# Optimization experiments

Measured on AMD Instinct MI355X. Metric: run time of the kernel, lower is better.

The kernel has to match this reference:

```python
import jax, jax.numpy as jnp
import numpy as np
from jax import lax

B, T, V, D, HD, H = 64, 256, 50000, 300, 1024, 512
L0, L1 = 13, 25


def setup_inputs() -> dict:
    key = jax.random.key(0)
    ks = list(jax.random.split(key, 24))
    lengths = jnp.concatenate([jnp.array([T]), jax.random.randint(ks[0], (B - 1,), T // 2, T + 1)])
    ids = jax.random.randint(ks[1], (B, T), 1, V)
    pos = jnp.arange(T)[None, :]
    word_batch = jnp.where(pos < lengths[:, None], ids, 0)
    def nrm(k, shape, s):
        return jax.random.normal(k, shape, dtype=jnp.float32) * s
    sc = 1.0 / float(np.sqrt(H))
    return dict(
        word_batch=word_batch,
        emb=nrm(ks[2], (V, D), 0.1),
        lstm0_wih=nrm(ks[3], (2, 4 * H, D), sc),
        lstm0_whh=nrm(ks[4], (2, 4 * H, H), sc),
        lstm0_b=nrm(ks[5], (2, 4 * H), sc),
        lstm1_wih=nrm(ks[6], (2, 4 * H, HD), sc),
        lstm1_whh=nrm(ks[7], (2, 4 * H, H), sc),
        lstm1_b=nrm(ks[8], (2, 4 * H), sc),
        head0_w=nrm(ks[9], (L0, HD), 0.02),
        head0_b=jnp.zeros((L0,), jnp.float32),
        head1_w=nrm(ks[10], (L1, HD + 1), 0.02),
        head1_b=jnp.zeros((L1,), jnp.float32),
        crf0_start=nrm(ks[11], (L0,), 0.1),
        crf0_end=nrm(ks[12], (L0,), 0.1),
        crf0_trans=nrm(ks[13], (L0, L0), 0.1),
        crf1_start=nrm(ks[14], (L1,), 0.1),
        crf1_end=nrm(ks[15], (L1,), 0.1),
        crf1_trans=nrm(ks[16], (L1, L1), 0.1),
    )


def reverse_padded(x, lengths):
    # reverse each sequence within its valid length; zeros in the padded tail
    Tn = x.shape[1]
    idx = lengths[:, None] - 1 - jnp.arange(Tn)[None, :]  # [B,T]
    valid = idx >= 0
    g = jnp.take_along_axis(x, jnp.clip(idx, 0)[:, :, None], axis=1)
    return jnp.where(valid[:, :, None], g, 0.0)


def lstm_scan(x, mask, w_ih, w_hh, b):
    # one direction; PyTorch gate order i,f,g,o. Packed-sequence semantics via mask
    Bn = x.shape[0]
    Hn = w_hh.shape[-1]
    xp = jnp.einsum('btd,gd->btg', x, w_ih) + b  # [B,T,4H]
    def step(carry, inp):
        h, c = carry
        gx, m = inp
        g = gx + h @ w_hh.T
        i, f, gg, o = jnp.split(g, 4, axis=-1)
        c_new = jax.nn.sigmoid(f) * c + jax.nn.sigmoid(i) * jnp.tanh(gg)
        h_new = jax.nn.sigmoid(o) * jnp.tanh(c_new)
        m2 = m[:, None]
        h = jnp.where(m2, h_new, h)
        c = jnp.where(m2, c_new, c)
        return (h, c), h * m2
    z = jnp.zeros((Bn, Hn), x.dtype)
    _, ys = lax.scan(step, (z, z), (xp.transpose(1, 0, 2), mask.T))
    return ys.transpose(1, 0, 2)


def bilstm_layer(x, mask, lengths, wih, whh, b):
    f = lstm_scan(x, mask, wih[0], whh[0], b[0])
    r = lstm_scan(reverse_padded(x, lengths), mask, wih[1], whh[1], b[1])
    return jnp.concatenate([f, reverse_padded(r, lengths)], axis=-1)


def viterbi(em, mask, start, end, trans):
    # torchcrf-style Viterbi decode with mask; identity-backpointers on padded steps
    Bn, Tn, Ln = em.shape
    score = start + em[:, 0]  # [B,L]
    iden = jnp.arange(Ln)[None, :]
    def step(score, inp):
        e, m = inp
        br = score[:, :, None] + trans[None]      # [B,Lprev,Lnext]
        nsc = jnp.max(br, axis=1) + e
        idx = jnp.argmax(br, axis=1)
        m2 = m[:, None]
        idx = jnp.where(m2, idx, iden)
        score = jnp.where(m2, nsc, score)
        return score, idx
    score, hist = lax.scan(step, score, (em[:, 1:].transpose(1, 0, 2), mask[:, 1:].T))
    final = score + end
    last = jnp.argmax(final, axis=-1)  # [B]
    best = jnp.max(final, axis=-1)
    def back(tag, h):
        prev = jnp.take_along_axis(h, tag[:, None], axis=1)[:, 0]
        return prev, prev
    _, prevs = lax.scan(back, last, hist, reverse=True)  # [T-1,B]
    tags = jnp.concatenate([prevs, last[None]], axis=0).T  # [B,T]
    return jnp.where(mask, tags, 0), best


def reference(word_batch, emb, lstm0_wih, lstm0_whh, lstm0_b, lstm1_wih, lstm1_whh, lstm1_b,
              head0_w, head0_b, head1_w, head1_b,
              crf0_start, crf0_end, crf0_trans, crf1_start, crf1_end, crf1_trans):
    mask = word_batch > 0
    lengths = mask.sum(axis=1)
    x = emb[word_batch]                                  # [B,T,D]
    out = bilstm_layer(x, mask, lengths, lstm0_wih, lstm0_whh, lstm0_b)
    out = bilstm_layer(out, mask, lengths, lstm1_wih, lstm1_whh, lstm1_b)  # [B,T,HD]
    em0 = out @ head0_w.T + head0_b
    tags0, _ = viterbi(em0, mask, crf0_start, crf0_end, crf0_trans)
    # extend: concat previous decoded tags (padded with 0) as an extra float channel
    ext = jnp.concatenate([out, tags0.astype(jnp.float32)[:, :, None]], axis=-1)
    em1 = ext @ head1_w.T + head1_b
    tags1, _ = viterbi(em1, mask, crf1_start, crf1_end, crf1_trans)
    return jnp.stack([tags0, tags1]), lengths
```

## Files before the change

### kernel.cpp

```cpp
#include <hip/hip_runtime.h>
#include <math.h>

#define B_ 64
#define T_ 256
#define D_ 300
#define H_ 512
#define G4_ 2048
#define HD_ 1024
#define CH_ 64
#define KP0 320

typedef short s8v __attribute__((ext_vector_type(8)));
typedef float f32x4 __attribute__((ext_vector_type(4)));
typedef __attribute__((address_space(1))) const char GChar;
typedef __attribute__((address_space(3))) char LChar;

#define HSWZ(lby, b) ((lby) ^ ((size_t)((b) & 15) << 4))

__device__ inline unsigned short f2bf_rne(float f) {
  unsigned u = __builtin_bit_cast(unsigned, f);
  unsigned r = (u + 0x7fff + ((u >> 16) & 1)) >> 16;
  return (unsigned short)r;
}
__device__ inline float bf2f(unsigned short h) {
  unsigned u = ((unsigned)h) << 16;
  return __builtin_bit_cast(float, u);
}

__device__ inline float fsig(float x) { return 1.f / (1.f + __expf(-x)); }
__device__ inline float ftanh(float x) { return 2.f / (1.f + __expf(-2.f * x)) - 1.f; }

__global__ void k_lengths(const int* __restrict__ word, int* __restrict__ lens,
                          int* __restrict__ out_len) {
  __shared__ int s[256];
  int b = blockIdx.x, t = threadIdx.x;
  s[t] = (word[b * T_ + t] > 0) ? 1 : 0;
  __syncthreads();
  for (int off = 128; off > 0; off >>= 1) {
    if (t < off) s[t] += s[t + off];
    __syncthreads();
  }
  if (t == 0) { lens[b] = s[0]; out_len[b] = s[0]; }
}

__global__ void k_embed_bf(const int* __restrict__ word, const float* __restrict__ emb,
                           unsigned short* __restrict__ xHi, unsigned short* __restrict__ xLo) {
  const int C8 = KP0 / 8;
  int idx = blockIdx.x * blockDim.x + threadIdx.x;
  if (idx >= T_ * B_ * C8) return;
  int d8 = idx % C8;
  int row = idx / C8;
  int b = row % B_, t = row / B_;
  int w = word[b * T_ + t];
  unsigned short hh[8], ll[8];
#pragma unroll
  for (int e = 0; e < 8; e++) {
    int d = d8 * 8 + e;
    float f = (d < D_) ? emb[(size_t)w * D_ + d] : 0.f;
    hh[e] = f2bf_rne(f);
    ll[e] = f2bf_rne(f - bf2f(hh[e]));
  }
  size_t o = (size_t)row * KP0 + d8 * 8;
  ((ushort4*)(xHi + o))[0] = make_ushort4(hh[0], hh[1], hh[2], hh[3]);
  ((ushort4*)(xHi + o))[1] = make_ushort4(hh[4], hh[5], hh[6], hh[7]);
  ((ushort4*)(xLo + o))[0] = make_ushort4(ll[0], ll[1], ll[2], ll[3]);
  ((ushort4*)(xLo + o))[1] = make_ushort4(ll[4], ll[5], ll[6], ll[7]);
}

__global__ void k_split(const float* __restrict__ w, unsigned short* __restrict__ hi,
                        unsigned short* __restrict__ lo, int n) {
  int i = blockIdx.x * blockDim.x + threadIdx.x;
  if (i >= n) return;
  float f = w[i];
  unsigned short h = f2bf_rne(f);
  hi[i] = h;
  lo[i] = f2bf_rne(f - bf2f(h));
}

template <int KP>
__global__ void k_splitw(const float* __restrict__ w, unsigned short* __restrict__ hi,
                         unsigned short* __restrict__ lo, int K) {
  const int C8 = KP / 8;
  int idx = blockIdx.x * blockDim.x + threadIdx.x;
  if (idx >= 2 * G4_ * C8) return;
  int d8 = idx % C8;
  int row = idx / C8;
  unsigned short hh[8], ll[8];
#pragma unroll
  for (int e = 0; e < 8; e++) {
    int d = d8 * 8 + e;
    float f = (d < K) ? w[(size_t)row * K + d] : 0.f;
    hh[e] = f2bf_rne(f);
    ll[e] = f2bf_rne(f - bf2f(hh[e]));
  }
  size_t o = (size_t)row * KP + d8 * 8;
  ((ushort4*)(hi + o))[0] = make_ushort4(hh[0], hh[1], hh[2], hh[3]);
  ((ushort4*)(hi + o))[1] = make_ushort4(hh[4], hh[5], hh[6], hh[7]);
  ((ushort4*)(lo + o))[0] = make_ushort4(ll[0], ll[1], ll[2], ll[3]);
  ((ushort4*)(lo + o))[1] = make_ushort4(ll[4], ll[5], ll[6], ll[7]);
}

template <int KSTEPS>
__global__ __launch_bounds__(256) void k_projg(
    const unsigned short* __restrict__ sHi, const unsigned short* __restrict__ sLo,
    const unsigned short* __restrict__ wHi, const unsigned short* __restrict__ wLo,
    const float* __restrict__ bias, const int* __restrict__ lens,
    float* __restrict__ xpf, float* __restrict__ xpr, int t0,
    const char* __restrict__ zpage) {
  const int KP = KSTEPS * 64;
  int mb = blockIdx.x, nb = blockIdx.y, rev = blockIdx.z;
  int tid = threadIdx.x;
  int w = tid >> 6, lane = tid & 63, lm = lane & 15;
  int wm = w >> 1, wn = w & 1;

  __shared__ char lds[65536];

  const char* aHp[4]; const char* aLp[4]; const char* bHp[4]; const char* bLp[4];
  int c16 = tid & 7;
#pragma unroll
  for (int it = 0; it < 4; it++) {
    int row = it * 32 + (tid >> 3);
    int sw = (c16 * 16) ^ ((row & 7) << 4);
    int grow = mb * 128 + row;
    int b = grow & 63, tl = grow >> 6;
    long srow;
    if (!rev) srow = (long)(t0 + tl) * B_ + b;
    else {
      int tp = lens[b] - 1 - (t0 + tl);
      srow = (tp >= 0) ? ((long)tp * B_ + b) : -1;
    }
    if (srow >= 0) {
      aHp[it] = (const char*)sHi + (size_t)srow * (KP * 2) + sw;
      aLp[it] = (const char*)sLo + (size_t)srow * (KP * 2) + sw;
    } else {
      aHp[it] = zpage + sw;
      aLp[it] = zpage + sw;
    }
    int col = nb * 128 + row;
    size_t wrow = (size_t)rev * G4_ + col;
    bHp[it] = (const char*)wHi + wrow * (KP * 2) + sw;
    bLp[it] = (const char*)wLo + wrow * (KP * 2) + sw;
  }

  f32x4 acc[4][4];
#pragma unroll
  for (int mi = 0; mi < 4; mi++)
#pragma unroll
    for (int ni = 0; ni < 4; ni++) {
      f32x4 z = {0.f, 0.f, 0.f, 0.f};
      acc[mi][ni] = z;
    }

  for (int ks = 0; ks < KSTEPS; ks++) {
    if (ks) __syncthreads();
    int so = ks * 128;
#pragma unroll
    for (int it = 0; it < 4; it++) {
      int o = it * 4096 + tid * 16;
      __builtin_amdgcn_global_load_lds((GChar*)(aHp[it] + so), (LChar*)(lds + o), 16, 0, 0);
      __builtin_amdgcn_global_load_lds((GChar*)(aLp[it] + so), (LChar*)(lds + 16384 + o), 16, 0, 0);
      __builtin_amdgcn_global_load_lds((GChar*)(bHp[it] + so), (LChar*)(lds + 32768 + o), 16, 0, 0);
      __builtin_amdgcn_global_load_lds((GChar*)(bLp[it] + so), (LChar*)(lds + 49152 + o), 16, 0, 0);
    }
    __syncthreads();
#pragma unroll
    for (int ki = 0; ki < 2; ki++) {
      int kb = ki * 64 + (lane >> 4) * 16;
      s8v ahf[4], alf[4], bhf[4], blf[4];
#pragma unroll
      for (int mi = 0; mi < 4; mi++) {
        int row = wm * 64 + mi * 16 + lm;
        int p = row * 128 + (kb ^ ((row & 7) << 4));
        ahf[mi] = *(const s8v*)(lds + p);
        alf[mi] = *(const s8v*)(lds + 16384 + p);
      }
#pragma unroll
      for (int ni = 0; ni < 4; ni++) {
        int row = wn * 64 + ni * 16 + lm;
        int p = row * 128 + (kb ^ ((row & 7) << 4));
        bhf[ni] = *(const s8v*)(lds + 32768 + p);
        blf[ni] = *(const s8v*)(lds + 49152 + p);
      }
#pragma unroll
      for (int mi = 0; mi < 4; mi++)
#pragma unroll
        for (int ni = 0; ni < 4; ni++) {
          acc[mi][ni] = __builtin_amdgcn_mfma_f32_16x16x32_bf16(ahf[mi], bhf[ni], acc[mi][ni], 0, 0, 0);
          acc[mi][ni] = __builtin_amdgcn_mfma_f32_16x16x32_bf16(alf[mi], bhf[ni], acc[mi][ni], 0, 0, 0);
          acc[mi][ni] = __builtin_amdgcn_mfma_f32_16x16x32_bf16(ahf[mi], blf[ni], acc[mi][ni], 0, 0, 0);
        }
    }
  }

  int tl = mb * 2 + wm;
  float* xpo = (rev ? xpr : xpf) + (size_t)tl * G4_ * B_;
#pragma unroll
  for (int ni = 0; ni < 4; ni++) {
    int col = nb * 128 + wn * 64 + ni * 16 + lm;
    float bv = bias[rev * G4_ + col];
    f32x4 bvv = {bv, bv, bv, bv};
#pragma unroll
    for (int mi = 0; mi < 4; mi++) {
      int b0 = mi * 16 + (lane >> 4) * 4;
      f32x4 v = acc[mi][ni] + bvv;
      *(f32x4*)(xpo + (size_t)col * B_ + b0) = v;
    }
  }
}

__global__ __launch_bounds__(512, 2) void k_lstm_chunk(
    const unsigned short* __restrict__ whh_hi, const unsigned short* __restrict__ whh_lo,
    const float* __restrict__ xpf, const float* __restrict__ xpr,
    const int* __restrict__ lens,
    unsigned short* __restrict__ hhi, unsigned short* __restrict__ hlo,
    float* __restrict__ cbuf,
    float* __restrict__ outF, unsigned short* __restrict__ oHi,
    unsigned short* __restrict__ oLo, int t0, int tbase, int mode,
    unsigned* __restrict__ flags) {
  int wg = blockIdx.x;
  int dir = wg >> 5;
  int u0 = (wg & 31) * 16;
  int tid = threadIdx.x;
  int w8 = tid >> 6;
  int g = w8 >> 1;
  int hh = w8 & 1;
  int lane = tid & 63;
  int lm = lane & 15;
  int kb = (lane >> 4) * 16;
  int n = g * H_ + u0 + lm;

  const unsigned short* Whi = whh_hi + (size_t)dir * G4_ * H_;
  const unsigned short* Wlo = whh_lo + (size_t)dir * G4_ * H_;
  const float* xpb = (dir == 0) ? xpf : xpr;

  __shared__ char lbuf[131072];
  float* glx = (float*)lbuf;

  s8v bh[16], bl[16];
#pragma unroll
  for (int kt = 0; kt < 16; kt++) {
    bh[kt] = *(const s8v*)(Whi + (size_t)n * H_ + kt * 32 + (kb >> 1));
    bl[kt] = *(const s8v*)(Wlo + (size_t)n * H_ + kt * 32 + (kb >> 1));
  }

  int eb = tid & 63;
  int uq = tid >> 6;
  int len = lens[eb];
  size_t lby = (size_t)eb * 1024 + (size_t)(u0 + uq * 2) * 2;
  size_t pby = HSWZ(lby, eb);
  size_t coff = ((size_t)dir * B_ + eb) * H_ + u0 + uq * 2;
  float2 cv2 = *(const float2*)(cbuf + coff);
  float creg[2] = {cv2.x, cv2.y};

  float xq[8];
#pragma unroll
  for (int q2 = 0; q2 < 8; q2++) {
    int gg = q2 >> 1, qq = q2 & 1;
    xq[q2] = xpb[(size_t)(gg * H_ + u0 + uq * 2 + qq) * B_ + eb];
  }

  {
    int pp = t0 & 1;
    const char* sH = (const char*)(hhi + (size_t)(pp * 2 + dir) * B_ * H_);
    const char* sL = (const char*)(hlo + (size_t)(pp * 2 + dir) * B_ * H_);
    int sof = w8 * 8192 + lane * 16;
#pragma unroll
    for (int it = 0; it < 8; it++) {
      __builtin_amdgcn_global_load_lds((GChar*)(sH + sof + it * 1024),
                                       (LChar*)(lbuf + sof + it * 1024), 16, 0, 16);
      __builtin_amdgcn_global_load_lds((GChar*)(sL + sof + it * 1024),
                                       (LChar*)(lbuf + 65536 + sof + it * 1024), 16, 0, 16);
    }
  }

  for (int tl = 0; tl < CH_; tl++) {
    int t = t0 + tl;
    int pp = t & 1;
    const char* srcHi = (const char*)(hhi + (size_t)(pp * 2 + dir) * B_ * H_);
    const char* srcLo = (const char*)(hlo + (size_t)(pp * 2 + dir) * B_ * H_);
    char* dstHi = (char*)(hhi + (size_t)((pp ^ 1) * 2 + dir) * B_ * H_);
    char* dstLo = (char*)(hlo + (size_t)((pp ^ 1) * 2 + dir) * B_ * H_);

    __syncthreads();

    f32x4 aH[2], aX[2];
#pragma unroll
    for (int b2 = 0; b2 < 2; b2++) {
      f32x4 z = {0.f, 0.f, 0.f, 0.f};
      aH[b2] = z; aX[b2] = z;
    }
#pragma unroll
    for (int kt = 0; kt < 16; kt++) {
#pragma unroll
      for (int b2 = 0; b2 < 2; b2++) {
        int row = (hh * 2 + b2) * 16 + lm;
        int p = (row * 1024 + kt * 64 + kb) ^ ((lm & 15) << 4);
        s8v ah = *(const s8v*)(lbuf + p);
        s8v al = *(const s8v*)(lbuf + 65536 + p);
        aH[b2] = __builtin_amdgcn_mfma_f32_16x16x32_bf16(ah, bh[kt], aH[b2], 0, 0, 0);
        aX[b2] = __builtin_amdgcn_mfma_f32_16x16x32_bf16(al, bh[kt], aX[b2], 0, 0, 0);
        aX[b2] = __builtin_amdgcn_mfma_f32_16x16x32_bf16(ah, bl[kt], aX[b2], 0, 0, 0);
      }
    }
    __syncthreads();
#pragma unroll
    for (int b2 = 0; b2 < 2; b2++) {
#pragma unroll
      for (int jj = 0; jj < 4; jj++) {
        int brow = (hh * 2 + b2) * 16 + (lane >> 4) * 4 + jj;
        glx[(g * 16 + lm) * 65 + brow] = aH[b2][jj] + aX[b2][jj];
      }
    }
    __syncthreads();

    bool active = (t < len);
    float hn[2];
    ushort2 hi2, lo2;
    if (active) {
#pragma unroll
      for (int q = 0; q < 2; q++) {
        int ul = uq * 2 + q;
        float iv = glx[(0 * 16 + ul) * 65 + eb] + xq[0 * 2 + q];
        float fv = glx[(1 * 16 + ul) * 65 + eb] + xq[1 * 2 + q];
        float gv = glx[(2 * 16 + ul) * 65 + eb] + xq[2 * 2 + q];
        float ov = glx[(3 * 16 + ul) * 65 + eb] + xq[3 * 2 + q];
        float cn = fsig(fv) * creg[q] + fsig(iv) * ftanh(gv);
        creg[q] = cn;
        hn[q] = fsig(ov) * ftanh(cn);
      }
      unsigned short h0 = f2bf_rne(hn[0]); unsigned short l0 = f2bf_rne(hn[0] - bf2f(h0));
      unsigned short h1 = f2bf_rne(hn[1]); unsigned short l1 = f2bf_rne(hn[1] - bf2f(h1));
      hi2.x = h0; hi2.y = h1;
      lo2.x = l0; lo2.y = l1;
      __hip_atomic_store((unsigned*)(dstHi + pby), __builtin_bit_cast(unsigned, hi2),
                         __ATOMIC_RELAXED, __HIP_MEMORY_SCOPE_AGENT);
      __hip_atomic_store((unsigned*)(dstLo + pby), __builtin_bit_cast(unsigned, lo2),
                         __ATOMIC_RELAXED, __HIP_MEMORY_SCOPE_AGENT);
    } else {
      unsigned vh = __hip_atomic_load((const unsigned*)(srcHi + pby),
                                      __ATOMIC_RELAXED, __HIP_MEMORY_SCOPE_AGENT);
      unsigned vl = __hip_atomic_load((const unsigned*)(srcLo + pby),
                                      __ATOMIC_RELAXED, __HIP_MEMORY_SCOPE_AGENT);
      __hip_atomic_store((unsigned*)(dstHi + pby), vh,
                         __ATOMIC_RELAXED, __HIP_MEMORY_SCOPE_AGENT);
      __hip_atomic_store((unsigned*)(dstLo + pby), vl,
                         __ATOMIC_RELAXED, __HIP_MEMORY_SCOPE_AGENT);
    }

    auto do_out = [&]() {
      if (active) {
        size_t orow = (dir == 0) ? ((size_t)t * B_ + eb) : ((size_t)(len - 1 - t) * B_ + eb);
        size_t ocol = (dir == 0) ? (size_t)(u0 + uq * 2) : (size_t)(H_ + u0 + uq * 2);
        if (mode == 0) {
          *(ushort2*)(oHi + orow * HD_ + ocol) = hi2;
          *(ushort2*)(oLo + orow * HD_ + ocol) = lo2;
        } else {
          float2 hv; hv.x = hn[0]; hv.y = hn[1];
          *(float2*)(outF + orow * HD_ + ocol) = hv;
        }
      } else if (dir == 0) {
        size_t o = ((size_t)t * B_ + eb) * HD_ + u0 + uq * 2;
        if (mode == 0) {
          ushort2 z2; z2.x = z2.y = 0;
          *(ushort2*)(oHi + o) = z2;
          *(ushort2*)(oLo + o) = z2;
        } else {
          float2 z; z.x = z.y = 0.f;
          *(float2*)(outF + o) = z;
        }
      }
    };

    if (tl != CH_ - 1) {
      unsigned target = (unsigned)(tbase + t + 1);
      __syncthreads();
      if (tid == 0)
        __hip_atomic_store(flags + wg * 16, target, __ATOMIC_RELAXED, __HIP_MEMORY_SCOPE_AGENT);
      do_out();
#pragma unroll
      for (int q2 = 0; q2 < 8; q2++) {
        int gg = q2 >> 1, qq = q2 & 1;
        xq[q2] = xpb[(size_t)(tl + 1) * G4_ * B_ + (size_t)(gg * H_ + u0 + uq * 2 + qq) * B_ + eb];
      }
      if (tid < 32) {
        const unsigned* p = flags + (dir * 32 + tid) * 16;
        while (true) {
          unsigned v = __hip_atomic_load(p, __ATOMIC_RELAXED, __HIP_MEMORY_SCOPE_AGENT);
          if (__all((int)(v >= target))) break;
        }
      }
      __syncthreads();
      {
        int np = (t + 1) & 1;
        const char* sH = (const char*)(hhi + (size_t)(np * 2 + dir) * B_ * H_);
        const char* sL = (const char*)(hlo + (size_t)(np * 2 + dir) * B_ * H_);
        int sof = w8 * 8192 + lane * 16;
#pragma unroll
        for (int it = 0; it < 8; it++) {
          __builtin_amdgcn_global_load_lds((GChar*)(sH + sof + it * 1024),
                                           (LChar*)(lbuf + sof + it * 1024), 16, 0, 16);
          __builtin_amdgcn_global_load_lds((GChar*)(sL + sof + it * 1024),
                                           (LChar*)(lbuf + 65536 + sof + it * 1024), 16, 0, 16);
        }
      }
    } else {
      do_out();
    }
  }
  *(float2*)(cbuf + coff) = *(const float2*)creg;
}

__global__ void k_em0(const float* __restrict__ o, const float* __restrict__ w,
                      const float* __restrict__ bias, float* __restrict__ em) {
  int gt = blockIdx.x * blockDim.x + threadIdx.x;
  int wid = gt >> 6;
  int lane = threadIdx.x & 63;
  if (wid >= T_ * B_) return;
  const float* row = o + (size_t)wid * HD_;
  float r[16];
#pragma unroll
  for (int q = 0; q < 16; q++) r[q] = row[lane + 64 * q];
  for (int c = 0; c < 13; c++) {
    const float* wr = w + (size_t)c * HD_;
    float p = 0.f;
#pragma unroll
    for (int q = 0; q < 16; q++) p += r[q] * wr[lane + 64 * q];
    for (int off = 32; off > 0; off >>= 1) p += __shfl_down(p, off);
    if (lane == 0) em[(size_t)wid * 16 + c] = p + bias[c];
  }
}

__global__ void k_em1(const float* __restrict__ o, const float* __restrict__ w,
                      const float* __restrict__ bias, const int* __restrict__ tags0,
                      float* __restrict__ em) {
  int gt = blockIdx.x * blockDim.x + threadIdx.x;
  int wid = gt >> 6;
  int lane = threadIdx.x & 63;
  if (wid >= T_ * B_) return;
  int t = wid / B_, b = wid % B_;
  float tag = (float)tags0[b * T_ + t];
  const float* row = o + (size_t)wid * HD_;
  float r[16];
#pragma unroll
  for (int q = 0; q < 16; q++) r[q] = row[lane + 64 * q];
  for (int c = 0; c < 25; c++) {
    const float* wr = w + (size_t)c * 1025;
    float p = 0.f;
#pragma unroll
    for (int q = 0; q < 16; q++) p += r[q] * wr[lane + 64 * q];
    for (int off = 32; off > 0; off >>= 1) p += __shfl_down(p, off);
    if (lane == 0) em[(size_t)wid * 32 + c] = p + wr[1024] * tag + bias[c];
  }
}

template <int L, int LD>
__global__ void k_viterbi(const float* __restrict__ em, const int* __restrict__ lens,
                          const float* __restrict__ startv, const float* __restrict__ endv,
                          const float* __restrict__ trans, int* __restrict__ tags) {
  int b = blockIdx.x;
  int j = threadIdx.x;
  __shared__ float sc[L];
  __shared__ float trT[L * L];
  __shared__ int hist[T_ * LD];
  int len = lens[b];
  if (j < L) {
    sc[j] = startv[j] + em[(size_t)b * LD + j];
    for (int i = 0; i < L; i++) trT[j * L + i] = trans[i * L + j];
  }
  __syncthreads();
  for (int t = 1; t < len; t++) {
    float nv = 0.f; int bi = 0;
    if (j < L) {
      float best = sc[0] + trT[j * L + 0];
      for (int i = 1; i < L; i++) {
        float v = sc[i] + trT[j * L + i];
        if (v > best) { best = v; bi = i; }
      }
      nv = best + em[((size_t)t * B_ + b) * LD + j];
      hist[t * LD + j] = bi;
    }
    __syncthreads();
    if (j < L) sc[j] = nv;
    __syncthreads();
  }
  if (j == 0) {
    float best = sc[0] + endv[0]; int bi = 0;
    for (int i = 1; i < L; i++) {
      float v = sc[i] + endv[i];
      if (v > best) { best = v; bi = i; }
    }
    int tag = bi;
    tags[b * T_ + (len - 1)] = tag;
    for (int t = len - 2; t >= 0; t--) {
      tag = hist[(t + 1) * LD + tag];
      tags[b * T_ + t] = tag;
    }
    for (int t = len; t < T_; t++) tags[b * T_ + t] = 0;
  }
}

extern "C" void kernel_launch(void* const* d_in, const int* in_sizes, int n_in,
                              void* d_out, int out_size, void* d_ws, size_t ws_size,
                              hipStream_t stream) {
  const int*   word = (const int*)d_in[0];
  const float* emb  = (const float*)d_in[1];
  const float* w0ih = (const float*)d_in[2];
  const float* w0hh = (const float*)d_in[3];
  const float* b0   = (const float*)d_in[4];
  const float* w1ih = (const float*)d_in[5];
  const float* w1hh = (const float*)d_in[6];
  const float* b1   = (const float*)d_in[7];
  const float* h0w  = (const float*)d_in[8];
  const float* h0b  = (const float*)d_in[9];
  const float* h1w  = (const float*)d_in[10];
  const float* h1b  = (const float*)d_in[11];
  const float* c0s  = (const float*)d_in[12];
  const float* c0e  = (const float*)d_in[13];
  const float* c0t  = (const float*)d_in[14];
  const float* c1s  = (const float*)d_in[15];
  const float* c1e  = (const float*)d_in[16];
  const float* c1t  = (const float*)d_in[17];

  int* out_tags0 = (int*)d_out;
  int* out_tags1 = out_tags0 + B_ * T_;
  int* out_len   = out_tags1 + B_ * T_;

  char* ws = (char*)d_ws;
  size_t off = 0;
  auto alloc = [&](size_t bytes) -> void* {
    void* p = ws + off;
    off += (bytes + 255) & ~(size_t)255;
    return p;
  };
  int*   lens  = (int*)alloc(B_ * 4);
  unsigned* sync = (unsigned*)alloc(4096);
  char*  zpage = (char*)alloc(4096);
  unsigned short* xHi = (unsigned short*)alloc((size_t)T_ * B_ * KP0 * 2);
  unsigned short* xLo = (unsigned short*)alloc((size_t)T_ * B_ * KP0 * 2);
  unsigned short* oHi = (unsigned short*)alloc((size_t)T_ * B_ * HD_ * 2);
  unsigned short* oLo = (unsigned short*)alloc((size_t)T_ * B_ * HD_ * 2);
  float* out1  = (float*)alloc((size_t)T_ * B_ * HD_ * 4);
  float* xpf   = (float*)alloc((size_t)CH_ * B_ * G4_ * 4);
  float* xpr   = (float*)alloc((size_t)CH_ * B_ * G4_ * 4);
  unsigned short* hhi = (unsigned short*)alloc((size_t)2 * 2 * B_ * H_ * 2);
  unsigned short* hlo = (unsigned short*)alloc((size_t)2 * 2 * B_ * H_ * 2);
  float* cbuf  = (float*)alloc((size_t)2 * B_ * H_ * 4);
  unsigned short* w0hh_hi = (unsigned short*)alloc((size_t)2 * G4_ * H_ * 2);
  unsigned short* w0hh_lo = (unsigned short*)alloc((size_t)2 * G4_ * H_ * 2);
  unsigned short* w1hh_hi = (unsigned short*)alloc((size_t)2 * G4_ * H_ * 2);
  unsigned short* w1hh_lo = (unsigned short*)alloc((size_t)2 * G4_ * H_ * 2);
  unsigned short* w0ih_hi = (unsigned short*)alloc((size_t)2 * G4_ * KP0 * 2);
  unsigned short* w0ih_lo = (unsigned short*)alloc((size_t)2 * G4_ * KP0 * 2);
  unsigned short* w1ih_hi = (unsigned short*)alloc((size_t)2 * G4_ * HD_ * 2);
  unsigned short* w1ih_lo = (unsigned short*)alloc((size_t)2 * G4_ * HD_ * 2);
  float* em0   = (float*)alloc((size_t)T_ * B_ * 16 * 4);
  float* em1   = (float*)alloc((size_t)T_ * B_ * 32 * 4);
  (void)ws_size; (void)in_sizes; (void)n_in; (void)out_size;

  hipMemsetAsync(sync, 0, 4096, stream);
  hipMemsetAsync(zpage, 0, 4096, stream);

  k_lengths<<<B_, 256, 0, stream>>>(word, lens, out_len);
  {
    int total = T_ * B_ * (KP0 / 8);
    k_embed_bf<<<(total + 255) / 256, 256, 0, stream>>>(word, emb, xHi, xLo);
  }
  {
    int n = 2 * G4_ * H_;
    k_split<<<(n + 255) / 256, 256, 0, stream>>>(w0hh, w0hh_hi, w0hh_lo, n);
    k_split<<<(n + 255) / 256, 256, 0, stream>>>(w1hh, w1hh_hi, w1hh_lo, n);
    int n0 = 2 * G4_ * (KP0 / 8);
    k_splitw<KP0><<<(n0 + 255) / 256, 256, 0, stream>>>(w0ih, w0ih_hi, w0ih_lo, D_);
    int n1 = 2 * G4_ * (HD_ / 8);
    k_splitw<HD_><<<(n1 + 255) / 256, 256, 0, stream>>>(w1ih, w1ih_hi, w1ih_lo, HD_);
  }

  for (int layer = 0; layer < 2; layer++) {
    const unsigned short* sHi = (layer == 0) ? xHi : oHi;
    const unsigned short* sLo = (layer == 0) ? xLo : oLo;
    const unsigned short* wiHi = (layer == 0) ? w0ih_hi : w1ih_hi;
    const unsigned short* wiLo = (layer == 0) ? w0ih_lo : w1ih_lo;
    const float* bb  = (layer == 0) ? b0 : b1;
    const unsigned short* whi = (layer == 0) ? w0hh_hi : w1hh_hi;
    const unsigned short* wlo = (layer == 0) ? w0hh_lo : w1hh_lo;
    hipMemsetAsync(hhi, 0, (size_t)2 * 2 * B_ * H_ * 2, stream);
    hipMemsetAsync(hlo, 0, (size_t)2 * 2 * B_ * H_ * 2, stream);
    hipMemsetAsync(cbuf, 0, (size_t)2 * B_ * H_ * 4, stream);
    if (layer == 0) {
      hipMemsetAsync(oHi, 0, (size_t)T_ * B_ * HD_ * 2, stream);
      hipMemsetAsync(oLo, 0, (size_t)T_ * B_ * HD_ * 2, stream);
    } else {
      hipMemsetAsync(out1, 0, (size_t)T_ * B_ * HD_ * 4, stream);
    }
    for (int cch = 0; cch < T_ / CH_; cch++) {
      dim3 pg(CH_ * B_ / 128, G4_ / 128, 2);
      if (layer == 0)
        k_projg<KP0 / 64><<<pg, 256, 0, stream>>>(sHi, sLo, wiHi, wiLo, bb, lens,
                                                  xpf, xpr, cch * CH_, zpage);
      else
        k_projg<HD_ / 64><<<pg, 256, 0, stream>>>(sHi, sLo, wiHi, wiLo, bb, lens,
                                                  xpf, xpr, cch * CH_, zpage);
      k_lstm_chunk<<<64, 512, 0, stream>>>(whi, wlo, xpf, xpr, lens, hhi, hlo,
                                           cbuf, out1, oHi, oLo,
                                           cch * CH_, layer * T_, layer, sync);
    }
  }

  k_em0<<<(T_ * B_) / 4, 256, 0, stream>>>(out1, h0w, h0b, em0);
  k_viterbi<13, 16><<<B_, 64, 0, stream>>>(em0, lens, c0s, c0e, c0t, out_tags0);
  k_em1<<<(T_ * B_) / 4, 256, 0, stream>>>(out1, h1w, h1b, out_tags0, em1);
  k_viterbi<25, 32><<<B_, 64, 0, stream>>>(em1, lens, c1s, c1e, c1t, out_tags1);
}
```

Baseline: 4.469 ms.

## Double LSTM recurrent block to 1024 threads, one batch tile per wave

The recurrent LSTM kernel now launches 1024 threads per block instead of 512. Each of the 16 waves computes a single 16-row batch tile of the h·Whh MFMA product rather than two, which halves the serial MFMA chain per wave on the latency-bound recurrence and halves the per-wave LDS staging loads. Only the first 512 threads run the gate epilogue, the state updates and the output writes. The cost is more idle threads during the epilogue, heavier barriers over 16 waves, and register pressure from keeping the Whh fragments in registers in every wave under the new launch bounds.

```diff
diff --git a/kernel.cpp b/kernel.cpp
--- a/kernel.cpp
+++ b/kernel.cpp
@@ -208,7 +208,7 @@
   }
 }
 
-__global__ __launch_bounds__(512, 2) void k_lstm_chunk(
+__global__ __launch_bounds__(1024, 4) void k_lstm_chunk(
     const unsigned short* __restrict__ whh_hi, const unsigned short* __restrict__ whh_lo,
     const float* __restrict__ xpf, const float* __restrict__ xpr,
     const int* __restrict__ lens,
@@ -221,9 +221,9 @@
   int dir = wg >> 5;
   int u0 = (wg & 31) * 16;
   int tid = threadIdx.x;
-  int w8 = tid >> 6;
-  int g = w8 >> 1;
-  int hh = w8 & 1;
+  int w16 = tid >> 6;
+  int g = w16 >> 2;
+  int bt = w16 & 3;
   int lane = tid & 63;
   int lm = lane & 15;
   int kb = (lane >> 4) * 16;
@@ -244,28 +244,34 @@
   }
 
   int eb = tid & 63;
-  int uq = tid >> 6;
+  int uq = (tid >> 6) & 7;
+  bool epi = (tid < 512);
   int len = lens[eb];
   size_t lby = (size_t)eb * 1024 + (size_t)(u0 + uq * 2) * 2;
   size_t pby = HSWZ(lby, eb);
   size_t coff = ((size_t)dir * B_ + eb) * H_ + u0 + uq * 2;
-  float2 cv2 = *(const float2*)(cbuf + coff);
-  float creg[2] = {cv2.x, cv2.y};
+  float creg[2] = {0.f, 0.f};
+  if (epi) {
+    float2 cv2 = *(const float2*)(cbuf + coff);
+    creg[0] = cv2.x; creg[1] = cv2.y;
+  }
 
   float xq[8];
-#pragma unroll
-  for (int q2 = 0; q2 < 8; q2++) {
-    int gg = q2 >> 1, qq = q2 & 1;
-    xq[q2] = xpb[(size_t)(gg * H_ + u0 + uq * 2 + qq) * B_ + eb];
+  if (epi) {
+#pragma unroll
+    for (int q2 = 0; q2 < 8; q2++) {
+      int gg = q2 >> 1, qq = q2 & 1;
+      xq[q2] = xpb[(size_t)(gg * H_ + u0 + uq * 2 + qq) * B_ + eb];
+    }
   }
 
   {
     int pp = t0 & 1;
     const char* sH = (const char*)(hhi + (size_t)(pp * 2 + dir) * B_ * H_);
     const char* sL = (const char*)(hlo + (size_t)(pp * 2 + dir) * B_ * H_);
-    int sof = w8 * 8192 + lane * 16;
-#pragma unroll
-    for (int it = 0; it < 8; it++) {
+    int sof = w16 * 4096 + lane * 16;
+#pragma unroll
+    for (int it = 0; it < 4; it++) {
       __builtin_amdgcn_global_load_lds((GChar*)(sH + sof + it * 1024),
                                        (LChar*)(lbuf + sof + it * 1024), 16, 0, 16);
       __builtin_amdgcn_global_load_lds((GChar*)(sL + sof + it * 1024),
@@ -283,37 +289,30 @@
 
     __syncthreads();
 
-    f32x4 aH[2], aX[2];
-#pragma unroll
-    for (int b2 = 0; b2 < 2; b2++) {
+    f32x4 aH, aX;
+    {
       f32x4 z = {0.f, 0.f, 0.f, 0.f};
-      aH[b2] = z; aX[b2] = z;
+      aH = z; aX = z;
     }
 #pragma unroll
     for (int kt = 0; kt < 16; kt++) {
-#pragma unroll
-      for (int b2 = 0; b2 < 2; b2++) {
-        int row = (hh * 2 + b2) * 16 + lm;
-        int p = (row * 1024 + kt * 64 + kb) ^ ((lm & 15) << 4);
-        s8v ah = *(const s8v*)(lbuf + p);
-        s8v al = *(const s8v*)(lbuf + 65536 + p);
-        aH[b2] = __builtin_amdgcn_mfma_f32_16x16x32_bf16(ah, bh[kt], aH[b2], 0, 0, 0);
-        aX[b2] = __builtin_amdgcn_mfma_f32_16x16x32_bf16(al, bh[kt], aX[b2], 0, 0, 0);
-        aX[b2] = __builtin_amdgcn_mfma_f32_16x16x32_bf16(ah, bl[kt], aX[b2], 0, 0, 0);
-      }
+      int row = bt * 16 + lm;
+      int p = (row * 1024 + kt * 64 + kb) ^ ((lm & 15) << 4);
+      s8v ah = *(const s8v*)(lbuf + p);
+      s8v al = *(const s8v*)(lbuf + 65536 + p);
+      aH = __builtin_amdgcn_mfma_f32_16x16x32_bf16(ah, bh[kt], aH, 0, 0, 0);
+      aX = __builtin_amdgcn_mfma_f32_16x16x32_bf16(al, bh[kt], aX, 0, 0, 0);
+      aX = __builtin_amdgcn_mfma_f32_16x16x32_bf16(ah, bl[kt], aX, 0, 0, 0);
     }
     __syncthreads();
 #pragma unroll
-    for (int b2 = 0; b2 < 2; b2++) {
-#pragma unroll
-      for (int jj = 0; jj < 4; jj++) {
-        int brow = (hh * 2 + b2) * 16 + (lane >> 4) * 4 + jj;
-        glx[(g * 16 + lm) * 65 + brow] = aH[b2][jj] + aX[b2][jj];
-      }
+    for (int jj = 0; jj < 4; jj++) {
+      int brow = bt * 16 + (lane >> 4) * 4 + jj;
+      glx[(g * 16 + lm) * 65 + brow] = aH[jj] + aX[jj];
     }
     __syncthreads();
 
-    bool active = (t < len);
+    bool active = epi && (t < len);
     float hn[2];
     ushort2 hi2, lo2;
     if (active) {
@@ -336,7 +335,7 @@
                          __ATOMIC_RELAXED, __HIP_MEMORY_SCOPE_AGENT);
       __hip_atomic_store((unsigned*)(dstLo + pby), __builtin_bit_cast(unsigned, lo2),
                          __ATOMIC_RELAXED, __HIP_MEMORY_SCOPE_AGENT);
-    } else {
+    } else if (epi) {
       unsigned vh = __hip_atomic_load((const unsigned*)(srcHi + pby),
                                       __ATOMIC_RELAXED, __HIP_MEMORY_SCOPE_AGENT);
       unsigned vl = __hip_atomic_load((const unsigned*)(srcLo + pby),
@@ -348,6 +347,7 @@
     }
 
     auto do_out = [&]() {
+      if (!epi) return;
       if (active) {
         size_t orow = (dir == 0) ? ((size_t)t * B_ + eb) : ((size_t)(len - 1 - t) * B_ + eb);
         size_t ocol = (dir == 0) ? (size_t)(u0 + uq * 2) : (size_t)(H_ + u0 + uq * 2);
@@ -377,10 +377,12 @@
       if (tid == 0)
         __hip_atomic_store(flags + wg * 16, target, __ATOMIC_RELAXED, __HIP_MEMORY_SCOPE_AGENT);
       do_out();
-#pragma unroll
-      for (int q2 = 0; q2 < 8; q2++) {
-        int gg = q2 >> 1, qq = q2 & 1;
-        xq[q2] = xpb[(size_t)(tl + 1) * G4_ * B_ + (size_t)(gg * H_ + u0 + uq * 2 + qq) * B_ + eb];
+      if (epi) {
+#pragma unroll
+        for (int q2 = 0; q2 < 8; q2++) {
+          int gg = q2 >> 1, qq = q2 & 1;
+          xq[q2] = xpb[(size_t)(tl + 1) * G4_ * B_ + (size_t)(gg * H_ + u0 + uq * 2 + qq) * B_ + eb];
+        }
       }
       if (tid < 32) {
         const unsigned* p = flags + (dir * 32 + tid) * 16;
@@ -394,9 +396,9 @@
         int np = (t + 1) & 1;
         const char* sH = (const char*)(hhi + (size_t)(np * 2 + dir) * B_ * H_);
         const char* sL = (const char*)(hlo + (size_t)(np * 2 + dir) * B_ * H_);
-        int sof = w8 * 8192 + lane * 16;
-#pragma unroll
-        for (int it = 0; it < 8; it++) {
+        int sof = w16 * 4096 + lane * 16;
+#pragma unroll
+        for (int it = 0; it < 4; it++) {
           __builtin_amdgcn_global_load_lds((GChar*)(sH + sof + it * 1024),
                                            (LChar*)(lbuf + sof + it * 1024), 16, 0, 16);
           __builtin_amdgcn_global_load_lds((GChar*)(sL + sof + it * 1024),
@@ -407,7 +409,7 @@
       do_out();
     }
   }
-  *(float2*)(cbuf + coff) = *(const float2*)creg;
+  if (epi) *(float2*)(cbuf + coff) = *(const float2*)creg;
 }
 
 __global__ void k_em0(const float* __restrict__ o, const float* __restrict__ w,
@@ -600,9 +602,9 @@
       else
         k_projg<HD_ / 64><<<pg, 256, 0, stream>>>(sHi, sLo, wiHi, wiLo, bb, lens,
                                                   xpf, xpr, cch * CH_, zpage);
-      k_lstm_chunk<<<64, 512, 0, stream>>>(whi, wlo, xpf, xpr, lens, hhi, hlo,
-                                           cbuf, out1, oHi, oLo,
-                                           cch * CH_, layer * T_, layer, sync);
+      k_lstm_chunk<<<64, 1024, 0, stream>>>(whi, wlo, xpf, xpr, lens, hhi, hlo,
+                                            cbuf, out1, oHi, oLo,
+                                            cch * CH_, layer * T_, layer, sync);
     }
   }
 
```

Result: slower. 7.340 ms (+64.2%).
